# Kernel optimization log

Measured on AMD Instinct MI355X. Metric: run time of the kernel, lower is better.

The kernel has to match this reference:

```python
import jax, jax.numpy as jnp
import numpy as np
import math

B, N, M, DK, H = 2, 2048, 2048, 512, 512  # input_v == hidden_size == H


def _lin(x, w, b):
    # torch Linear: y = x @ W.T + b, w: [out, in]
    return jnp.einsum('bnd,od->bno', x, w) + b


def setup_inputs() -> dict:
    key = jax.random.key(0)
    ks = jax.random.split(key, 20)
    s = 0.02
    d = {
        'KEY': jax.random.normal(ks[0], (B, N, DK), jnp.float32),
        'VALUE': jax.random.normal(ks[1], (B, N, H), jnp.float32),
        'QUERY': jax.random.normal(ks[2], (B, M, DK), jnp.float32),
        # W MLP: input_k -> hidden -> hidden -> input_k
        'W1_w': jax.random.normal(ks[3], (H, DK), jnp.float32) * s,
        'W1_b': jnp.zeros((H,), jnp.float32),
        'W2_w': jax.random.normal(ks[4], (H, H), jnp.float32) * s,
        'W2_b': jnp.zeros((H,), jnp.float32),
        'W3_w': jax.random.normal(ks[5], (DK, H), jnp.float32) * s,
        'W3_b': jnp.zeros((DK,), jnp.float32),
        # Wv MLP: input_v -> hidden -> hidden -> hidden
        'V1_w': jax.random.normal(ks[6], (H, H), jnp.float32) * s,
        'V1_b': jnp.zeros((H,), jnp.float32),
        'V2_w': jax.random.normal(ks[7], (H, H), jnp.float32) * s,
        'V2_b': jnp.zeros((H,), jnp.float32),
        'V3_w': jax.random.normal(ks[8], (H, H), jnp.float32) * s,
        'V3_b': jnp.zeros((H,), jnp.float32),
        # Wo: hidden -> input_v
        'Wo_w': jax.random.normal(ks[9], (H, H), jnp.float32) * s,
        'Wo_b': jnp.zeros((H,), jnp.float32),
    }
    return d


def reference(KEY, VALUE, QUERY, W1_w, W1_b, W2_w, W2_b, W3_w, W3_b,
              V1_w, V1_b, V2_w, V2_b, V3_w, V3_b, Wo_w, Wo_b):
    def mlp(x, w1, b1, w2, b2, w3, b3):
        h = jax.nn.relu(_lin(x, w1, b1))
        h = jax.nn.relu(_lin(h, w2, b2))
        return _lin(h, w3, b3)

    Wk = mlp(KEY, W1_w, W1_b, W2_w, W2_b, W3_w, W3_b)      # [b,n,dk]
    Wq = mlp(QUERY, W1_w, W1_b, W2_w, W2_b, W3_w, W3_b)    # [b,m,dk]
    Wv = mlp(VALUE, V1_w, V1_b, V2_w, V2_b, V3_w, V3_b)    # [b,n,h]

    KEY_s = KEY * Wk
    QUERY_s = QUERY * Wq
    VALUE_s = VALUE * Wv

    d_wk = KEY_s.shape[-1]
    dist = jnp.einsum('bij,bkj->bik', KEY_s, QUERY_s) / math.sqrt(d_wk)  # [b,n,m]
    weights = jax.nn.softmax(-(dist ** 2) * 0.5, axis=1)  # softmax over keys
    context = jnp.einsum('bik,bij->bkj', weights, VALUE_s)  # [b,m,h]
    # dropout is identity in eval mode
    return _lin(context, Wo_w, Wo_b)  # [b,m,input_v]
```

## Files before the change

### kernel.cpp

```cpp
#include <hip/hip_runtime.h>
#include <math.h>

typedef unsigned short u16;
typedef unsigned int u32;
typedef __attribute__((ext_vector_type(8))) short short8;
typedef __attribute__((ext_vector_type(4))) float f32x4;
typedef __attribute__((ext_vector_type(4))) u16 u16x4;

__device__ __forceinline__ void gload16(const void* g, void* l) {
    __builtin_amdgcn_global_load_lds(
        (__attribute__((address_space(1))) u32*)g,
        (__attribute__((address_space(3))) u32*)l, 16, 0, 0);
}

__device__ __forceinline__ u16 f2bf_rne(float v) {
    u32 u = __builtin_bit_cast(u32, v);
    return (u16)((u + 0x7FFFu + ((u >> 16) & 1u)) >> 16);
}
__device__ __forceinline__ float bf2f(u16 h) {
    u32 u = ((u32)h) << 16;
    return __builtin_bit_cast(float, u);
}
__device__ __forceinline__ void splt(float v, u16& h, u16& l) {
    h = f2bf_rne(v);
    l = f2bf_rne(v - bf2f(h));
}

enum { EP_RELU, EP_MUL };
enum { EP_PART };

template<int EP>
__global__ __launch_bounds__(256)
void mlp2(const u16* __restrict__ Ah, const u16* __restrict__ Al,
          const u16* __restrict__ BHkq, const u16* __restrict__ BLkq,
          const u16* __restrict__ BHv, const u16* __restrict__ BLv,
          const float* __restrict__ bias_kq, const float* __restrict__ bias_v,
          const float* __restrict__ Xk, const float* __restrict__ Xq,
          const float* __restrict__ Xv,
          u16* __restrict__ Ch, u16* __restrict__ Cl,
          u16* __restrict__ vtH, u16* __restrict__ vtL)
{
    __shared__ u16 LAh[2][128 * 32];
    __shared__ u16 LAl[2][128 * 32];
    __shared__ u16 LBh[2][128 * 32];
    __shared__ u16 LBl[2][128 * 32];

    const int tid = threadIdx.x;
    const int lane = tid & 63;
    const int wave = tid >> 6;
    const int wr = wave >> 1, wc = wave & 1;
    const int fr = lane & 15, kg = lane >> 4;

    const int L = blockIdx.y * 4 + blockIdx.x;
    const int xcd = L & 7;
    const int i = L >> 3;
    const int panel = xcd * 12 + (i >> 2);
    const int m0 = panel * 128, n0 = (i & 3) * 128;
    const int sec = panel >> 5;

    const u16* Bh = (sec == 2) ? BHv : BHkq;
    const u16* Bl = (sec == 2) ? BLv : BLkq;
    const float* bias = (sec == 2) ? bias_v : bias_kq;

    f32x4 acc[4][4];
    #pragma unroll
    for (int a = 0; a < 4; ++a)
        #pragma unroll
        for (int j = 0; j < 4; ++j)
            acc[a][j] = (f32x4){0.f, 0.f, 0.f, 0.f};

    auto STAGE = [&](int buf, int kk) {
        #pragma unroll
        for (int h = 0; h < 2; ++h) {
            int c = h * 256 + tid;
            long so = (long)(m0 + (c >> 2)) * 512 + kk + (c & 3) * 8;
            gload16(Ah + so, &LAh[buf][c * 8]);
        }
        #pragma unroll
        for (int h = 0; h < 2; ++h) {
            int c = h * 256 + tid;
            long so = (long)(m0 + (c >> 2)) * 512 + kk + (c & 3) * 8;
            gload16(Al + so, &LAl[buf][c * 8]);
        }
        #pragma unroll
        for (int h = 0; h < 2; ++h) {
            int c = h * 256 + tid;
            long so = (long)(n0 + (c >> 2)) * 512 + kk + (c & 3) * 8;
            gload16(Bh + so, &LBh[buf][c * 8]);
        }
        #pragma unroll
        for (int h = 0; h < 2; ++h) {
            int c = h * 256 + tid;
            long so = (long)(n0 + (c >> 2)) * 512 + kk + (c & 3) * 8;
            gload16(Bl + so, &LBl[buf][c * 8]);
        }
    };

    auto COMPUTE = [&](int buf) {
        short8 ah[4], al[4], bh[4], bl[4];
        #pragma unroll
        for (int a = 0; a < 4; ++a) {
            int off = (wr * 64 + a * 16 + fr) * 32 + kg * 8;
            ah[a] = *(const short8*)&LAh[buf][off];
            al[a] = *(const short8*)&LAl[buf][off];
        }
        #pragma unroll
        for (int j = 0; j < 4; ++j) {
            int off = (wc * 64 + j * 16 + fr) * 32 + kg * 8;
            bh[j] = *(const short8*)&LBh[buf][off];
            bl[j] = *(const short8*)&LBl[buf][off];
        }
        #pragma unroll
        for (int a = 0; a < 4; ++a)
            #pragma unroll
            for (int j = 0; j < 4; ++j) {
                acc[a][j] = __builtin_amdgcn_mfma_f32_16x16x32_bf16(ah[a], bh[j], acc[a][j], 0, 0, 0);
                acc[a][j] = __builtin_amdgcn_mfma_f32_16x16x32_bf16(ah[a], bl[j], acc[a][j], 0, 0, 0);
                acc[a][j] = __builtin_amdgcn_mfma_f32_16x16x32_bf16(al[a], bh[j], acc[a][j], 0, 0, 0);
            }
    };

    STAGE(0, 0);
    int cur = 0;
    for (int t = 0; t < 15; ++t) {
        STAGE(cur ^ 1, (t + 1) << 5);
        asm volatile("s_waitcnt vmcnt(8)" ::: "memory");
        __builtin_amdgcn_s_barrier();
        COMPUTE(cur);
        __builtin_amdgcn_s_barrier();
        cur ^= 1;
    }
    asm volatile("s_waitcnt vmcnt(0)" ::: "memory");
    __builtin_amdgcn_s_barrier();
    COMPUTE(cur);

    const float* X = (EP == EP_MUL) ? ((sec == 0) ? Xk : (sec == 1) ? Xq : Xv) : nullptr;

    #pragma unroll
    for (int a = 0; a < 4; ++a)
        #pragma unroll
        for (int j = 0; j < 4; ++j)
            #pragma unroll
            for (int r = 0; r < 4; ++r) {
                int row = m0 + wr * 64 + a * 16 + kg * 4 + r;
                int col = n0 + wc * 64 + j * 16 + fr;
                float v = acc[a][j][r] + bias[col];
                u16 h, l;
                if constexpr (EP == EP_RELU) {
                    v = fmaxf(v, 0.f);
                    splt(v, h, l);
                    long o = (long)row * 512 + col;
                    Ch[o] = h; Cl[o] = l;
                } else {
                    v *= X[(long)(row - (sec << 12)) * 512 + col];
                    splt(v, h, l);
                    if (sec < 2) {
                        long o = (long)row * 512 + col;
                        Ch[o] = h; Cl[o] = l;
                    } else {
                        int rb = row - 8192;
                        long o = (long)(rb >> 11) * 1048576 + (long)col * 2048 + (rb & 2047);
                        vtH[o] = h; vtL[o] = l;
                    }
                }
            }
}

__global__ __launch_bounds__(256)
void dist2(const u16* __restrict__ QH, const u16* __restrict__ QL,
           const u16* __restrict__ KH, const u16* __restrict__ KL,
           u16* __restrict__ S)
{
    __shared__ u16 LAh[2][128 * 32];
    __shared__ u16 LAl[2][128 * 32];
    __shared__ u16 LBh[2][128 * 32];
    __shared__ u16 LBl[2][128 * 32];

    const int tid = threadIdx.x;
    const int lane = tid & 63;
    const int wave = tid >> 6;
    const int wr = wave >> 1, wc = wave & 1;
    const int fr = lane & 15, kg = lane >> 4;

    const int L = (blockIdx.z * 16 + blockIdx.y) * 16 + blockIdx.x;
    const int xcd = L & 7;
    const int pos = L >> 3;
    const int b = xcd >> 2, quad = xcd & 3;
    const int mi = (quad >> 1) * 8 + (pos >> 3);
    const int ni = (quad & 1) * 8 + (pos & 7);
    const int m0 = mi * 128, n0 = ni * 128;

    const u16* Ah = QH + (long)b * 1048576;
    const u16* Al = QL + (long)b * 1048576;
    const u16* Bh = KH + (long)b * 1048576;
    const u16* Bl = KL + (long)b * 1048576;

    f32x4 acc[4][4];
    #pragma unroll
    for (int a = 0; a < 4; ++a)
        #pragma unroll
        for (int j = 0; j < 4; ++j)
            acc[a][j] = (f32x4){0.f, 0.f, 0.f, 0.f};

    auto STAGE = [&](int buf, int kk) {
        #pragma unroll
        for (int h = 0; h < 2; ++h) {
            int c = h * 256 + tid;
            long so = (long)(m0 + (c >> 2)) * 512 + kk + (c & 3) * 8;
            gload16(Ah + so, &LAh[buf][c * 8]);
        }
        #pragma unroll
        for (int h = 0; h < 2; ++h) {
            int c = h * 256 + tid;
            long so = (long)(m0 + (c >> 2)) * 512 + kk + (c & 3) * 8;
            gload16(Al + so, &LAl[buf][c * 8]);
        }
        #pragma unroll
        for (int h = 0; h < 2; ++h) {
            int c = h * 256 + tid;
            long so = (long)(n0 + (c >> 2)) * 512 + kk + (c & 3) * 8;
            gload16(Bh + so, &LBh[buf][c * 8]);
        }
        #pragma unroll
        for (int h = 0; h < 2; ++h) {
            int c = h * 256 + tid;
            long so = (long)(n0 + (c >> 2)) * 512 + kk + (c & 3) * 8;
            gload16(Bl + so, &LBl[buf][c * 8]);
        }
    };

    auto COMPUTE = [&](int buf) {
        short8 ah[4], al[4], bh[4], bl[4];
        #pragma unroll
        for (int a = 0; a < 4; ++a) {
            int off = (wr * 64 + a * 16 + fr) * 32 + kg * 8;
            ah[a] = *(const short8*)&LAh[buf][off];
            al[a] = *(const short8*)&LAl[buf][off];
        }
        #pragma unroll
        for (int j = 0; j < 4; ++j) {
            int off = (wc * 64 + j * 16 + fr) * 32 + kg * 8;
            bh[j] = *(const short8*)&LBh[buf][off];
            bl[j] = *(const short8*)&LBl[buf][off];
        }
        #pragma unroll
        for (int a = 0; a < 4; ++a)
            #pragma unroll
            for (int j = 0; j < 4; ++j) {
                acc[a][j] = __builtin_amdgcn_mfma_f32_16x16x32_bf16(ah[a], bh[j], acc[a][j], 0, 0, 0);
                acc[a][j] = __builtin_amdgcn_mfma_f32_16x16x32_bf16(ah[a], bl[j], acc[a][j], 0, 0, 0);
                acc[a][j] = __builtin_amdgcn_mfma_f32_16x16x32_bf16(al[a], bh[j], acc[a][j], 0, 0, 0);
            }
    };

    STAGE(0, 0);
    int cur = 0;
    for (int t = 0; t < 15; ++t) {
        STAGE(cur ^ 1, (t + 1) << 5);
        asm volatile("s_waitcnt vmcnt(8)" ::: "memory");
        __builtin_amdgcn_s_barrier();
        COMPUTE(cur);
        __builtin_amdgcn_s_barrier();
        cur ^= 1;
    }
    asm volatile("s_waitcnt vmcnt(0)" ::: "memory");
    __builtin_amdgcn_s_barrier();
    COMPUTE(cur);

    u16* Sb = S + (long)b * 8388608;
    #pragma unroll
    for (int a = 0; a < 4; ++a)
        #pragma unroll
        for (int j = 0; j < 4; ++j)
            #pragma unroll
            for (int r = 0; r < 4; ++r) {
                int row = m0 + wr * 64 + a * 16 + kg * 4 + r;
                int col = n0 + wc * 64 + j * 16 + fr;
                float v = acc[a][j][r];
                v = -(v * v) * (1.0f / 1024.0f);
                u16 h, l; splt(v, h, l);
                u16* p = Sb + (long)row * 4096 + col;
                p[0] = h; p[2048] = l;
            }
}

template<int EP>
__global__ __launch_bounds__(256)
void gemm_pf(int K, int nsl, int KS,
             const u16* __restrict__ Ah, const u16* __restrict__ Al, int lda, long sA,
             const u16* __restrict__ Bh, const u16* __restrict__ Bl, int ldb, long sB,
             float* __restrict__ Cf, int ldc, long sC)
{
    __shared__ u16 LAh[2][128 * 32];
    __shared__ u16 LAl[2][128 * 32];
    __shared__ u16 LBh[2][64 * 32];
    __shared__ u16 LBl[2][64 * 32];

    const int tid = threadIdx.x;
    const int lane = tid & 63;
    const int wave = tid >> 6;
    const int wr = wave >> 1, wc = wave & 1;
    const int fr = lane & 15, kg = lane >> 4;

    int bx, by, bz;
    {
        const int gx = gridDim.x, gy = gridDim.y;
        const int L = (blockIdx.z * gy + blockIdx.y) * gx + blockIdx.x;
        const int xcd = L & 7;
        const int i = L >> 3;
        const int P = gy * gridDim.z;
        const int ppx = P >> 3;
        bx = i % gx;
        const int panel = xcd * ppx + i / gx;
        by = panel % gy;
        bz = panel / gy;
    }

    const int b = bz / nsl;
    const int s = bz - b * nsl;
    const int k0 = s * KS;
    int k1 = k0 + KS; if (k1 > K) k1 = K;
    const int nt = (k1 - k0) >> 5;

    Ah += b * sA; Al += b * sA;
    Bh += b * sB; Bl += b * sB;
    const long cb = (long)bz * sC;

    const int m0 = by * 128, n0 = bx * 64;

    f32x4 acc[4][2];
    #pragma unroll
    for (int a = 0; a < 4; ++a)
        #pragma unroll
        for (int j = 0; j < 2; ++j)
            acc[a][j] = (f32x4){0.f, 0.f, 0.f, 0.f};

    auto STAGE = [&](int buf, int kk) {
        #pragma unroll
        for (int h = 0; h < 2; ++h) {
            int c = h * 256 + tid;
            long so = (long)(m0 + (c >> 2)) * lda + kk + (c & 3) * 8;
            gload16(Ah + so, &LAh[buf][c * 8]);
        }
        #pragma unroll
        for (int h = 0; h < 2; ++h) {
            int c = h * 256 + tid;
            long so = (long)(m0 + (c >> 2)) * lda + kk + (c & 3) * 8;
            gload16(Al + so, &LAl[buf][c * 8]);
        }
        {
            int c = tid;
            long so = (long)(n0 + (c >> 2)) * ldb + kk + (c & 3) * 8;
            gload16(Bh + so, &LBh[buf][c * 8]);
            gload16(Bl + so, &LBl[buf][c * 8]);
        }
    };

    auto COMPUTE = [&](int buf) {
        short8 ah[4], al[4], bh[2], bl[2];
        #pragma unroll
        for (int a = 0; a < 4; ++a) {
            int off = (wr * 64 + a * 16 + fr) * 32 + kg * 8;
            ah[a] = *(const short8*)&LAh[buf][off];
            al[a] = *(const short8*)&LAl[buf][off];
        }
        #pragma unroll
        for (int j = 0; j < 2; ++j) {
            int off = (wc * 32 + j * 16 + fr) * 32 + kg * 8;
            bh[j] = *(const short8*)&LBh[buf][off];
            bl[j] = *(const short8*)&LBl[buf][off];
        }
        #pragma unroll
        for (int a = 0; a < 4; ++a)
            #pragma unroll
            for (int j = 0; j < 2; ++j) {
                acc[a][j] = __builtin_amdgcn_mfma_f32_16x16x32_bf16(ah[a], bh[j], acc[a][j], 0, 0, 0);
                acc[a][j] = __builtin_amdgcn_mfma_f32_16x16x32_bf16(ah[a], bl[j], acc[a][j], 0, 0, 0);
                acc[a][j] = __builtin_amdgcn_mfma_f32_16x16x32_bf16(al[a], bh[j], acc[a][j], 0, 0, 0);
            }
    };

    STAGE(0, k0);
    int cur = 0;
    for (int t = 0; t < nt - 1; ++t) {
        STAGE(cur ^ 1, k0 + ((t + 1) << 5));
        asm volatile("s_waitcnt vmcnt(6)" ::: "memory");
        __builtin_amdgcn_s_barrier();
        COMPUTE(cur);
        __builtin_amdgcn_s_barrier();
        cur ^= 1;
    }
    asm volatile("s_waitcnt vmcnt(0)" ::: "memory");
    __builtin_amdgcn_s_barrier();
    COMPUTE(cur);

    #pragma unroll
    for (int a = 0; a < 4; ++a)
        #pragma unroll
        for (int j = 0; j < 2; ++j)
            #pragma unroll
            for (int r = 0; r < 4; ++r) {
                int row = m0 + wr * 64 + a * 16 + kg * 4 + r;
                int col = n0 + wc * 32 + j * 16 + fr;
                Cf[cb + (long)row * ldc + col] = acc[a][j][r];
            }
}

__global__ __launch_bounds__(256)
void softmax16(u16* __restrict__ S)
{
    long row = blockIdx.x;
    u16* hi = S + row * 4096;
    u16* lo = hi + 2048;
    int tid = threadIdx.x;
    int lane = tid & 63, w = tid >> 6;

    u16x4 h0 = ((u16x4*)hi)[tid * 2];
    u16x4 h1 = ((u16x4*)hi)[tid * 2 + 1];
    u16x4 l0 = ((u16x4*)lo)[tid * 2];
    u16x4 l1 = ((u16x4*)lo)[tid * 2 + 1];

    float v[8];
    #pragma unroll
    for (int i = 0; i < 4; ++i) {
        v[i]     = bf2f(h0[i]) + bf2f(l0[i]);
        v[4 + i] = bf2f(h1[i]) + bf2f(l1[i]);
    }

    float m = v[0];
    #pragma unroll
    for (int i = 1; i < 8; ++i) m = fmaxf(m, v[i]);
    #pragma unroll
    for (int o = 32; o; o >>= 1) m = fmaxf(m, __shfl_xor(m, o));

    __shared__ float redm[4];
    __shared__ float reds[4];
    if (lane == 0) redm[w] = m;
    __syncthreads();
    m = fmaxf(fmaxf(redm[0], redm[1]), fmaxf(redm[2], redm[3]));

    float s = 0.f;
    #pragma unroll
    for (int i = 0; i < 8; ++i) { v[i] = expf(v[i] - m); s += v[i]; }
    #pragma unroll
    for (int o = 32; o; o >>= 1) s += __shfl_xor(s, o);
    if (lane == 0) reds[w] = s;
    __syncthreads();
    s = reds[0] + reds[1] + reds[2] + reds[3];
    float inv = 1.0f / s;

    u16 h, l;
    #pragma unroll
    for (int i = 0; i < 4; ++i) {
        splt(v[i] * inv, h, l);     h0[i] = h; l0[i] = l;
        splt(v[4 + i] * inv, h, l); h1[i] = h; l1[i] = l;
    }
    ((u16x4*)hi)[tid * 2] = h0;
    ((u16x4*)hi)[tid * 2 + 1] = h1;
    ((u16x4*)lo)[tid * 2] = l0;
    ((u16x4*)lo)[tid * 2 + 1] = l1;
}

__global__ __launch_bounds__(256)
void split_w(const float* __restrict__ w0, const float* __restrict__ w1,
             const float* __restrict__ w2, const float* __restrict__ w3,
             const float* __restrict__ w4, const float* __restrict__ w5,
             const float* __restrict__ w6, u16* __restrict__ dst)
{
    int wi = blockIdx.y;
    const float* src;
    switch (wi) {
        case 0: src = w0; break; case 1: src = w1; break;
        case 2: src = w2; break; case 3: src = w3; break;
        case 4: src = w4; break; case 5: src = w5; break;
        default: src = w6; break;
    }
    u16* hi = dst + (long)wi * 524288;
    u16* lo = hi + 262144;
    int i = blockIdx.x * 256 + threadIdx.x;
    float4 v = ((const float4*)src)[i];
    u16x4 h4, l4; u16 h, l;
    splt(v.x, h, l); h4.x = h; l4.x = l;
    splt(v.y, h, l); h4.y = h; l4.y = l;
    splt(v.z, h, l); h4.z = h; l4.z = l;
    splt(v.w, h, l); h4.w = h; l4.w = l;
    ((u16x4*)hi)[i] = h4;
    ((u16x4*)lo)[i] = l4;
}

__global__ __launch_bounds__(256)
void split_in(const float* __restrict__ k, const float* __restrict__ q,
              const float* __restrict__ vv, u16* __restrict__ hi, u16* __restrict__ lo)
{
    int sec = blockIdx.y;
    const float* src = (sec == 0) ? k : (sec == 1) ? q : vv;
    long base4 = (long)sec * 524288;
    int i = blockIdx.x * 256 + threadIdx.x;
    float4 v = ((const float4*)src)[i];
    u16x4 h4, l4; u16 h, l;
    splt(v.x, h, l); h4.x = h; l4.x = l;
    splt(v.y, h, l); h4.y = h; l4.y = l;
    splt(v.z, h, l); h4.z = h; l4.z = l;
    splt(v.w, h, l); h4.w = h; l4.w = l;
    ((u16x4*)(hi))[base4 + i] = h4;
    ((u16x4*)(lo))[base4 + i] = l4;
}

__global__ __launch_bounds__(256)
void reduce_ctx(const float* __restrict__ P, u16* __restrict__ ctH, u16* __restrict__ ctL)
{
    int i4 = blockIdx.x * 256 + threadIdx.x;
    long e = (long)i4 * 4;
    int b = (int)(e >> 20);
    long r = e & ((1L << 20) - 1);
    const float* base = P + ((long)(b * 2) << 20) + r;
    float4 v0 = *(const float4*)base;
    float4 v1 = *(const float4*)(base + (1L << 20));
    u16x4 h4, l4; u16 h, l;
    splt(v0.x + v1.x, h, l); h4.x = h; l4.x = l;
    splt(v0.y + v1.y, h, l); h4.y = h; l4.y = l;
    splt(v0.z + v1.z, h, l); h4.z = h; l4.z = l;
    splt(v0.w + v1.w, h, l); h4.w = h; l4.w = l;
    ((u16x4*)ctH)[i4] = h4;
    ((u16x4*)ctL)[i4] = l4;
}

__global__ __launch_bounds__(256)
void reduce_out(const float* __restrict__ P, const float* __restrict__ bias,
                float* __restrict__ out)
{
    int i4 = blockIdx.x * 256 + threadIdx.x;
    long e = (long)i4 * 4;
    float4 a = ((const float4*)P)[i4];
    float4 c = ((const float4*)(P + 2097152))[i4];
    float4 bb = *(const float4*)(bias + (e & 511));
    float4 o;
    o.x = a.x + c.x + bb.x;
    o.y = a.y + c.y + bb.y;
    o.z = a.z + c.z + bb.z;
    o.w = a.w + c.w + bb.w;
    ((float4*)out)[i4] = o;
}

extern "C" void kernel_launch(void* const* d_in, const int* in_sizes, int n_in,
                              void* d_out, int out_size, void* d_ws, size_t ws_size,
                              hipStream_t stream)
{
    const float* KEY   = (const float*)d_in[0];
    const float* VALUE = (const float*)d_in[1];
    const float* QUERY = (const float*)d_in[2];
    const float* W1w = (const float*)d_in[3];
    const float* W1b = (const float*)d_in[4];
    const float* W2w = (const float*)d_in[5];
    const float* W2b = (const float*)d_in[6];
    const float* W3w = (const float*)d_in[7];
    const float* W3b = (const float*)d_in[8];
    const float* V1w = (const float*)d_in[9];
    const float* V1b = (const float*)d_in[10];
    const float* V2w = (const float*)d_in[11];
    const float* V2b = (const float*)d_in[12];
    const float* V3w = (const float*)d_in[13];
    const float* V3b = (const float*)d_in[14];
    const float* Wow = (const float*)d_in[15];
    const float* Wob = (const float*)d_in[16];
    float* out = (float*)d_out;

    const long SEC  = 2097152;
    const long FULL = 3 * SEC;

    u16* Wb = (u16*)d_ws;
    u16* B0p = Wb + 3670016;
    u16* cH = B0p;            u16* cL = B0p + FULL;
    u16* h1H = B0p + 6 * SEC; u16* h1L = B0p + 9 * SEC;
    u16* h2H = B0p + 12 * SEC; u16* h2L = B0p + 15 * SEC;
    u16* ksH = B0p;            u16* ksL = B0p + FULL;
    u16* qsH = B0p + SEC;
    u16* vtH = B0p + 2 * SEC;  u16* vtL = B0p + FULL + 2 * SEC;
    u16* sTu = B0p + 6 * SEC;
    float* Pctx = (float*)(B0p + 14 * SEC);
    u16* ctH = B0p;            u16* ctL = B0p + SEC;
    float* Pout = (float*)(B0p + 14 * SEC);

    u16* wH6 = Wb + 6L * 524288;
    u16* wL6 = wH6 + 262144;

    dim3 blk(256);

    split_w<<<dim3(256, 7), blk, 0, stream>>>(W1w, W2w, W3w, V1w, V2w, V3w, Wow, Wb);
    split_in<<<dim3(2048, 3), blk, 0, stream>>>(KEY, QUERY, VALUE, cH, cL);

    dim3 gL(4, 96, 1);
    mlp2<EP_RELU><<<gL, blk, 0, stream>>>(
        cH, cL, Wb, Wb + 262144, Wb + 3 * 524288, Wb + 3 * 524288 + 262144,
        W1b, V1b, nullptr, nullptr, nullptr, h1H, h1L, nullptr, nullptr);
    mlp2<EP_RELU><<<gL, blk, 0, stream>>>(
        h1H, h1L, Wb + 524288, Wb + 524288 + 262144, Wb + 4 * 524288, Wb + 4 * 524288 + 262144,
        W2b, V2b, nullptr, nullptr, nullptr, h2H, h2L, nullptr, nullptr);
    mlp2<EP_MUL><<<gL, blk, 0, stream>>>(
        h2H, h2L, Wb + 2 * 524288, Wb + 2 * 524288 + 262144, Wb + 5 * 524288, Wb + 5 * 524288 + 262144,
        W3b, V3b, KEY, QUERY, VALUE, ksH, ksL, vtH, vtL);

    dist2<<<dim3(16, 16, 2), blk, 0, stream>>>(qsH, qsH + FULL, ksH, ksL, sTu);

    softmax16<<<dim3(4096), blk, 0, stream>>>(sTu);

    gemm_pf<EP_PART><<<dim3(8, 16, 4), blk, 0, stream>>>(
        2048, 2, 1024,
        sTu, sTu + 2048, 4096, 8388608,
        vtH, vtL, 2048, 1048576,
        Pctx, 512, 1048576);

    reduce_ctx<<<dim3(2048), blk, 0, stream>>>(Pctx, ctH, ctL);

    gemm_pf<EP_PART><<<dim3(8, 32, 2), blk, 0, stream>>>(
        512, 2, 256,
        ctH, ctL, 512, 0,
        wH6, wL6, 512, 0,
        Pout, 512, 2097152);

    reduce_out<<<dim3(2048), blk, 0, stream>>>(Pout, Wob, out);
}
```

Baseline: 235.7 us.

## Narrow MLP GEMM tiles, transpose V separately, and deepen context split-K

The MLP GEMM tile drops from 128x128 to 128x64, which doubles the block count and halves the B-side LDS staging and accumulators. The scattered transposed write of the scaled VALUE output in the MLP epilogue is replaced by plain row-major stores followed by a dedicated LDS-tiled transpose kernel. The context GEMM moves from 2 to 3 K-splits (chunk 704), and reduce_ctx sums three partials; the workspace layout is rearranged to fit. The aim is better CU occupancy and coalesced stores, at the cost of an extra launch, an extra pass over V, and reloading the A tile more often.

```diff
diff --git a/kernel.cpp b/kernel.cpp
--- a/kernel.cpp
+++ b/kernel.cpp
@@ -31,19 +31,18 @@
 
 template<int EP>
 __global__ __launch_bounds__(256)
-void mlp2(const u16* __restrict__ Ah, const u16* __restrict__ Al,
-          const u16* __restrict__ BHkq, const u16* __restrict__ BLkq,
-          const u16* __restrict__ BHv, const u16* __restrict__ BLv,
-          const float* __restrict__ bias_kq, const float* __restrict__ bias_v,
-          const float* __restrict__ Xk, const float* __restrict__ Xq,
-          const float* __restrict__ Xv,
-          u16* __restrict__ Ch, u16* __restrict__ Cl,
-          u16* __restrict__ vtH, u16* __restrict__ vtL)
+void mlp_pf(const u16* __restrict__ Ah, const u16* __restrict__ Al,
+            const u16* __restrict__ BHkq, const u16* __restrict__ BLkq,
+            const u16* __restrict__ BHv, const u16* __restrict__ BLv,
+            const float* __restrict__ bias_kq, const float* __restrict__ bias_v,
+            const float* __restrict__ Xk, const float* __restrict__ Xq,
+            const float* __restrict__ Xv,
+            u16* __restrict__ Ch, u16* __restrict__ Cl)
 {
     __shared__ u16 LAh[2][128 * 32];
     __shared__ u16 LAl[2][128 * 32];
-    __shared__ u16 LBh[2][128 * 32];
-    __shared__ u16 LBl[2][128 * 32];
+    __shared__ u16 LBh[2][64 * 32];
+    __shared__ u16 LBl[2][64 * 32];
 
     const int tid = threadIdx.x;
     const int lane = tid & 63;
@@ -51,22 +50,22 @@
     const int wr = wave >> 1, wc = wave & 1;
     const int fr = lane & 15, kg = lane >> 4;
 
-    const int L = blockIdx.y * 4 + blockIdx.x;
+    const int L = blockIdx.y * 8 + blockIdx.x;
     const int xcd = L & 7;
     const int i = L >> 3;
-    const int panel = xcd * 12 + (i >> 2);
-    const int m0 = panel * 128, n0 = (i & 3) * 128;
+    const int panel = xcd * 12 + (i >> 3);
+    const int m0 = panel * 128, n0 = (i & 7) * 64;
     const int sec = panel >> 5;
 
     const u16* Bh = (sec == 2) ? BHv : BHkq;
     const u16* Bl = (sec == 2) ? BLv : BLkq;
     const float* bias = (sec == 2) ? bias_v : bias_kq;
 
-    f32x4 acc[4][4];
+    f32x4 acc[4][2];
     #pragma unroll
     for (int a = 0; a < 4; ++a)
         #pragma unroll
-        for (int j = 0; j < 4; ++j)
+        for (int j = 0; j < 2; ++j)
             acc[a][j] = (f32x4){0.f, 0.f, 0.f, 0.f};
 
     auto STAGE = [&](int buf, int kk) {
@@ -82,22 +81,16 @@
             long so = (long)(m0 + (c >> 2)) * 512 + kk + (c & 3) * 8;
             gload16(Al + so, &LAl[buf][c * 8]);
         }
-        #pragma unroll
-        for (int h = 0; h < 2; ++h) {
-            int c = h * 256 + tid;
+        {
+            int c = tid;
             long so = (long)(n0 + (c >> 2)) * 512 + kk + (c & 3) * 8;
             gload16(Bh + so, &LBh[buf][c * 8]);
-        }
-        #pragma unroll
-        for (int h = 0; h < 2; ++h) {
-            int c = h * 256 + tid;
-            long so = (long)(n0 + (c >> 2)) * 512 + kk + (c & 3) * 8;
             gload16(Bl + so, &LBl[buf][c * 8]);
         }
     };
 
     auto COMPUTE = [&](int buf) {
-        short8 ah[4], al[4], bh[4], bl[4];
+        short8 ah[4], al[4], bh[2], bl[2];
         #pragma unroll
         for (int a = 0; a < 4; ++a) {
             int off = (wr * 64 + a * 16 + fr) * 32 + kg * 8;
@@ -105,15 +98,15 @@
             al[a] = *(const short8*)&LAl[buf][off];
         }
         #pragma unroll
-        for (int j = 0; j < 4; ++j) {
-            int off = (wc * 64 + j * 16 + fr) * 32 + kg * 8;
+        for (int j = 0; j < 2; ++j) {
+            int off = (wc * 32 + j * 16 + fr) * 32 + kg * 8;
             bh[j] = *(const short8*)&LBh[buf][off];
             bl[j] = *(const short8*)&LBl[buf][off];
         }
         #pragma unroll
         for (int a = 0; a < 4; ++a)
             #pragma unroll
-            for (int j = 0; j < 4; ++j) {
+            for (int j = 0; j < 2; ++j) {
                 acc[a][j] = __builtin_amdgcn_mfma_f32_16x16x32_bf16(ah[a], bh[j], acc[a][j], 0, 0, 0);
                 acc[a][j] = __builtin_amdgcn_mfma_f32_16x16x32_bf16(ah[a], bl[j], acc[a][j], 0, 0, 0);
                 acc[a][j] = __builtin_amdgcn_mfma_f32_16x16x32_bf16(al[a], bh[j], acc[a][j], 0, 0, 0);
@@ -124,7 +117,7 @@
     int cur = 0;
     for (int t = 0; t < 15; ++t) {
         STAGE(cur ^ 1, (t + 1) << 5);
-        asm volatile("s_waitcnt vmcnt(8)" ::: "memory");
+        asm volatile("s_waitcnt vmcnt(6)" ::: "memory");
         __builtin_amdgcn_s_barrier();
         COMPUTE(cur);
         __builtin_amdgcn_s_barrier();
@@ -139,30 +132,20 @@
     #pragma unroll
     for (int a = 0; a < 4; ++a)
         #pragma unroll
-        for (int j = 0; j < 4; ++j)
+        for (int j = 0; j < 2; ++j)
             #pragma unroll
             for (int r = 0; r < 4; ++r) {
                 int row = m0 + wr * 64 + a * 16 + kg * 4 + r;
-                int col = n0 + wc * 64 + j * 16 + fr;
+                int col = n0 + wc * 32 + j * 16 + fr;
                 float v = acc[a][j][r] + bias[col];
-                u16 h, l;
                 if constexpr (EP == EP_RELU) {
                     v = fmaxf(v, 0.f);
-                    splt(v, h, l);
-                    long o = (long)row * 512 + col;
-                    Ch[o] = h; Cl[o] = l;
                 } else {
                     v *= X[(long)(row - (sec << 12)) * 512 + col];
-                    splt(v, h, l);
-                    if (sec < 2) {
-                        long o = (long)row * 512 + col;
-                        Ch[o] = h; Cl[o] = l;
-                    } else {
-                        int rb = row - 8192;
-                        long o = (long)(rb >> 11) * 1048576 + (long)col * 2048 + (rb & 2047);
-                        vtH[o] = h; vtL[o] = l;
-                    }
                 }
+                long o = (long)row * 512 + col;
+                u16 h, l; splt(v, h, l);
+                Ch[o] = h; Cl[o] = l;
             }
 }
 
@@ -462,6 +445,31 @@
 }
 
 __global__ __launch_bounds__(256)
+void transpose16(const u16* __restrict__ vH, const u16* __restrict__ vL,
+                 u16* __restrict__ tH, u16* __restrict__ tL)
+{
+    __shared__ float t[32][33];
+    int b = blockIdx.z;
+    int c0 = blockIdx.x * 32;
+    int r0 = blockIdx.y * 32;
+    int tx = threadIdx.x, ty = threadIdx.y;
+    #pragma unroll
+    for (int k = 0; k < 4; ++k) {
+        long idx = (long)(b * 2048 + r0 + ty + 8 * k) * 512 + c0 + tx;
+        t[ty + 8 * k][tx] = bf2f(vH[idx]) + bf2f(vL[idx]);
+    }
+    __syncthreads();
+    long ob = (long)b * 512 * 2048;
+    #pragma unroll
+    for (int k = 0; k < 4; ++k) {
+        float v = t[tx][ty + 8 * k];
+        u16 h, l; splt(v, h, l);
+        long o = ob + (long)(c0 + ty + 8 * k) * 2048 + r0 + tx;
+        tH[o] = h; tL[o] = l;
+    }
+}
+
+__global__ __launch_bounds__(256)
 void split_w(const float* __restrict__ w0, const float* __restrict__ w1,
              const float* __restrict__ w2, const float* __restrict__ w3,
              const float* __restrict__ w4, const float* __restrict__ w5,
@@ -513,14 +521,15 @@
     long e = (long)i4 * 4;
     int b = (int)(e >> 20);
     long r = e & ((1L << 20) - 1);
-    const float* base = P + ((long)(b * 2) << 20) + r;
+    const float* base = P + ((long)(b * 3) << 20) + r;
     float4 v0 = *(const float4*)base;
     float4 v1 = *(const float4*)(base + (1L << 20));
+    float4 v2 = *(const float4*)(base + (2L << 20));
     u16x4 h4, l4; u16 h, l;
-    splt(v0.x + v1.x, h, l); h4.x = h; l4.x = l;
-    splt(v0.y + v1.y, h, l); h4.y = h; l4.y = l;
-    splt(v0.z + v1.z, h, l); h4.z = h; l4.z = l;
-    splt(v0.w + v1.w, h, l); h4.w = h; l4.w = l;
+    splt(v0.x + v1.x + v2.x, h, l); h4.x = h; l4.x = l;
+    splt(v0.y + v1.y + v2.y, h, l); h4.y = h; l4.y = l;
+    splt(v0.z + v1.z + v2.z, h, l); h4.z = h; l4.z = l;
+    splt(v0.w + v1.w + v2.w, h, l); h4.w = h; l4.w = l;
     ((u16x4*)ctH)[i4] = h4;
     ((u16x4*)ctL)[i4] = l4;
 }
@@ -565,21 +574,22 @@
     const float* Wob = (const float*)d_in[16];
     float* out = (float*)d_out;
 
-    const long SEC  = 2097152;
+    const long SEC  = 4096L * 512;
     const long FULL = 3 * SEC;
 
     u16* Wb = (u16*)d_ws;
-    u16* B0p = Wb + 3670016;
-    u16* cH = B0p;            u16* cL = B0p + FULL;
-    u16* h1H = B0p + 6 * SEC; u16* h1L = B0p + 9 * SEC;
-    u16* h2H = B0p + 12 * SEC; u16* h2L = B0p + 15 * SEC;
-    u16* ksH = B0p;            u16* ksL = B0p + FULL;
-    u16* qsH = B0p + SEC;
-    u16* vtH = B0p + 2 * SEC;  u16* vtL = B0p + FULL + 2 * SEC;
-    u16* sTu = B0p + 6 * SEC;
-    float* Pctx = (float*)(B0p + 14 * SEC);
-    u16* ctH = B0p;            u16* ctL = B0p + SEC;
-    float* Pout = (float*)(B0p + 14 * SEC);
+    u16* cH = Wb + 3670016;
+    u16* cL = cH + FULL;
+    u16* R1 = cL + FULL;
+    u16* h1H = R1,            *h1L = R1 + FULL;
+    u16* h2H = R1 + 2 * FULL, *h2L = R1 + 3 * FULL;
+    u16* sTu = R1;
+    u16* vtH = R1 + 16777216;
+    u16* vtL = vtH + 2097152;
+    u16* ctH = R1 + 20971520;
+    u16* ctL = ctH + 2097152;
+    float* Pctx = (float*)cH;
+    float* Pout = (float*)cH;
 
     u16* wH6 = Wb + 6L * 524288;
     u16* wL6 = wH6 + 262144;
@@ -589,23 +599,29 @@
     split_w<<<dim3(256, 7), blk, 0, stream>>>(W1w, W2w, W3w, V1w, V2w, V3w, Wow, Wb);
     split_in<<<dim3(2048, 3), blk, 0, stream>>>(KEY, QUERY, VALUE, cH, cL);
 
-    dim3 gL(4, 96, 1);
-    mlp2<EP_RELU><<<gL, blk, 0, stream>>>(
+    dim3 gL(8, 96, 1);
+    mlp_pf<EP_RELU><<<gL, blk, 0, stream>>>(
         cH, cL, Wb, Wb + 262144, Wb + 3 * 524288, Wb + 3 * 524288 + 262144,
-        W1b, V1b, nullptr, nullptr, nullptr, h1H, h1L, nullptr, nullptr);
-    mlp2<EP_RELU><<<gL, blk, 0, stream>>>(
+        W1b, V1b, nullptr, nullptr, nullptr, h1H, h1L);
+    mlp_pf<EP_RELU><<<gL, blk, 0, stream>>>(
         h1H, h1L, Wb + 524288, Wb + 524288 + 262144, Wb + 4 * 524288, Wb + 4 * 524288 + 262144,
-        W2b, V2b, nullptr, nullptr, nullptr, h2H, h2L, nullptr, nullptr);
-    mlp2<EP_MUL><<<gL, blk, 0, stream>>>(
+        W2b, V2b, nullptr, nullptr, nullptr, h2H, h2L);
+    mlp_pf<EP_MUL><<<gL, blk, 0, stream>>>(
         h2H, h2L, Wb + 2 * 524288, Wb + 2 * 524288 + 262144, Wb + 5 * 524288, Wb + 5 * 524288 + 262144,
-        W3b, V3b, KEY, QUERY, VALUE, ksH, ksL, vtH, vtL);
-
-    dist2<<<dim3(16, 16, 2), blk, 0, stream>>>(qsH, qsH + FULL, ksH, ksL, sTu);
+        W3b, V3b, KEY, QUERY, VALUE, cH, cL);
+
+    transpose16<<<dim3(16, 64, 2), dim3(32, 8), 0, stream>>>(
+        cH + 2 * SEC, cL + 2 * SEC, vtH, vtL);
+
+    dist2<<<dim3(16, 16, 2), blk, 0, stream>>>(
+        cH + SEC, cL + SEC,
+        cH, cL,
+        sTu);
 
     softmax16<<<dim3(4096), blk, 0, stream>>>(sTu);
 
-    gemm_pf<EP_PART><<<dim3(8, 16, 4), blk, 0, stream>>>(
-        2048, 2, 1024,
+    gemm_pf<EP_PART><<<dim3(8, 16, 6), blk, 0, stream>>>(
+        2048, 3, 704,
         sTu, sTu + 2048, 4096, 8388608,
         vtH, vtL, 2048, 1048576,
         Pctx, 512, 1048576);
```

Result: faster. 214.2 us (-9.1%).
